# Optimization experiments

Hardware: AMD Instinct MI355X
Metric: run time of the kernel (lower is better)

## Reference

```python
import jax, jax.numpy as jnp
import numpy as np

DIM = 1024
MEM_DIM = 1024
BANK = 8192
B, S = 4, 4096
LN_EPS = 1e-5


def setup_inputs() -> dict:
    key = jax.random.key(0)
    ks = jax.random.split(key, 8)
    std_q = 1.0 / np.sqrt(DIM)
    std_m = 1.0 / np.sqrt(MEM_DIM)
    std_f = 1.0 / np.sqrt(DIM + MEM_DIM)
    return {
        "x": jax.random.normal(ks[0], (B, S, DIM), jnp.float32),
        "knowledge_bank": 0.02 * jax.random.normal(ks[1], (BANK, MEM_DIM), jnp.float32),
        "wq": std_q * jax.random.normal(ks[2], (MEM_DIM, DIM), jnp.float32),
        "bq": jnp.zeros((MEM_DIM,), jnp.float32),
        "wk": std_m * jax.random.normal(ks[3], (MEM_DIM, MEM_DIM), jnp.float32),
        "bk": jnp.zeros((MEM_DIM,), jnp.float32),
        "wv": std_m * jax.random.normal(ks[4], (DIM, MEM_DIM), jnp.float32),
        "bv": jnp.zeros((DIM,), jnp.float32),
        "wf": std_f * jax.random.normal(ks[5], (DIM, DIM + MEM_DIM), jnp.float32),
        "bf": jnp.zeros((DIM,), jnp.float32),
        "gamma": jnp.ones((DIM,), jnp.float32),
        "beta": jnp.zeros((DIM,), jnp.float32),
    }


def reference(x, knowledge_bank, wq, bq, wk, bk, wv, bv, wf, bf, gamma, beta):
    # queries: [B,S,MEM_DIM]; keys/values over the fixed bank: [BANK, *]
    queries = jnp.einsum("bsd,md->bsm", x, wq) + bq
    keys = jnp.einsum("nd,md->nm", knowledge_bank, wk) + bk
    values = jnp.einsum("nd,md->nm", knowledge_bank, wv) + bv
    scores = jnp.einsum("bsm,nm->bsn", queries, keys) / jnp.sqrt(
        jnp.asarray(MEM_DIM, x.dtype)
    )
    attn = jax.nn.softmax(scores, axis=-1)  # [B,S,BANK]
    retrieved = jnp.einsum("bsn,nd->bsd", attn, values)  # [B,S,DIM]
    combined = jnp.concatenate([x, retrieved], axis=-1)  # [B,S,2*DIM]
    out = jnp.einsum("bsc,dc->bsd", combined, wf) + bf
    h = out + x
    # LayerNorm over last dim, eps = 1e-5 (torch default)
    mu = jnp.mean(h, axis=-1, keepdims=True)
    var = jnp.mean(jnp.square(h - mu), axis=-1, keepdims=True)
    return (h - mu) * jax.lax.rsqrt(var + LN_EPS) * gamma + beta
```

## Files before the change

### kernel.cpp

```cpp
#include <hip/hip_runtime.h>


typedef __bf16 bf16;
typedef __bf16 bf16x4 __attribute__((ext_vector_type(4)));
typedef __bf16 bf16x8 __attribute__((ext_vector_type(8)));
typedef float f32x4 __attribute__((ext_vector_type(4)));

static __device__ __forceinline__ f32x4 mfma16(bf16x8 a, bf16x8 b, f32x4 c) {
  return __builtin_amdgcn_mfma_f32_16x16x32_bf16(a, b, c, 0, 0, 0);
}

#define GLDS16(gp, lp) __builtin_amdgcn_global_load_lds( \
    (const __attribute__((address_space(1))) void*)(gp), \
    (__attribute__((address_space(3))) void*)(lp), 16, 0, 0)

static __device__ __forceinline__ void xcd_swizzle(long& bm, long& bn) {
  const int nwg = (int)(gridDim.x * gridDim.y);
  int flat = (int)(blockIdx.y * gridDim.x + blockIdx.x);
  flat = (flat & 7) * (nwg >> 3) + (flat >> 3);
  bm = (long)(flat / (int)gridDim.x) * 128;
  bn = (long)(flat % (int)gridDim.x) * 128;
}

template<int EPI, int CONCAT>
__global__ __launch_bounds__(256, 3) void gemm_bb(
    const bf16* __restrict__ A, const bf16* __restrict__ A2,
    const bf16* __restrict__ W, const float* __restrict__ bias,
    const float* __restrict__ resid, float* __restrict__ L,
    void* __restrict__ Cout, int N, int K, int ldw)
{
  __shared__ bf16 As[128 * 64];
  __shared__ bf16 Bs[128 * 64];
  const int tid = threadIdx.x, lane = tid & 63, wid = tid >> 6;
  const int wm = (wid >> 1) * 64, wn = (wid & 1) * 64;
  const int quad = lane >> 4, l16 = lane & 15;
  long bm, bn;
  xcd_swizzle(bm, bn);

  int prow[4], pcg[4];
#pragma unroll
  for (int i = 0; i < 4; ++i) {
    int p = ((wid * 4 + i) << 6) + lane;
    prow[i] = p >> 3;
    pcg[i] = (p & 7) ^ (prow[i] & 7);
  }

  f32x4 acc[4][4] = {};

  for (int k0 = 0; k0 < K; k0 += 64) {
    const bf16* Asrc = (CONCAT && k0 >= 1024) ? A2 : A;
    const int kA = (CONCAT && k0 >= 1024) ? k0 - 1024 : k0;
    const int lda = CONCAT ? 1024 : K;
    __syncthreads();
#pragma unroll
    for (int i = 0; i < 4; ++i) {
      const bf16* ga = Asrc + (size_t)(bm + prow[i]) * lda + kA + pcg[i] * 8;
      GLDS16(ga, (char*)As + ((wid * 4 + i) << 10));
    }
#pragma unroll
    for (int i = 0; i < 4; ++i) {
      const bf16* gb = W + (size_t)(bn + prow[i]) * ldw + k0 + pcg[i] * 8;
      GLDS16(gb, (char*)Bs + ((wid * 4 + i) << 10));
    }
    __syncthreads();
#pragma unroll
    for (int kk = 0; kk < 2; ++kk) {
      bf16x8 af[4], bfv[4];
#pragma unroll
      for (int mt = 0; mt < 4; ++mt) {
        const int r = wm + mt * 16 + l16;
        af[mt] = *(const bf16x8*)((const char*)As + (r << 7)
                                  + ((((kk << 2) + quad) ^ (r & 7)) << 4));
      }
#pragma unroll
      for (int nt = 0; nt < 4; ++nt) {
        const int r = wn + nt * 16 + l16;
        bfv[nt] = *(const bf16x8*)((const char*)Bs + (r << 7)
                                   + ((((kk << 2) + quad) ^ (r & 7)) << 4));
      }
#pragma unroll
      for (int mt = 0; mt < 4; ++mt)
#pragma unroll
        for (int nt = 0; nt < 4; ++nt)
          acc[mt][nt] = mfma16(af[mt], bfv[nt], acc[mt][nt]);
    }
  }

#pragma unroll
  for (int mt = 0; mt < 4; ++mt) {
    const long row0 = bm + wm + mt * 16 + quad * 4;
    if (EPI == 2) {
      float rsum[4] = {0.f, 0.f, 0.f, 0.f};
#pragma unroll
      for (int nt = 0; nt < 4; ++nt) {
        const long col = bn + wn + nt * 16 + l16;
#pragma unroll
        for (int r = 0; r < 4; ++r) {
          float p = __expf(acc[mt][nt][r] * 0.03125f);
          rsum[r] += p;
          ((bf16*)Cout)[(size_t)(row0 + r) * N + col] = (bf16)p;
        }
      }
#pragma unroll
      for (int s = 1; s < 16; s <<= 1)
#pragma unroll
        for (int r = 0; r < 4; ++r) rsum[r] += __shfl_xor(rsum[r], s, 64);
      if (l16 == 0) {
#pragma unroll
        for (int r = 0; r < 4; ++r) atomicAdd(&L[row0 + r], rsum[r]);
      }
    } else {
#pragma unroll
      for (int nt = 0; nt < 4; ++nt) {
        const long col = bn + wn + nt * 16 + l16;
        const float bc = (EPI == 1) ? 0.f : bias[col];
#pragma unroll
        for (int r = 0; r < 4; ++r) {
          float v = acc[mt][nt][r] + ((EPI == 1) ? bias[row0 + r] : bc);
          if (EPI == 3) {
            v += resid[(size_t)(row0 + r) * 1024 + col];
            ((float*)Cout)[(size_t)(row0 + r) * N + col] = v;
          } else {
            ((bf16*)Cout)[(size_t)(row0 + r) * N + col] = (bf16)v;
          }
        }
      }
    }
  }
}

__global__ __launch_bounds__(512, 2) void pv_gemm(
    const bf16* __restrict__ P, const bf16* __restrict__ Vt,
    const float* __restrict__ L, bf16* __restrict__ Rb)
{
  __shared__ bf16 As[2][128 * 128];
  __shared__ bf16 Bs[2][128 * 128];
  const int tid = threadIdx.x, lane = tid & 63, wid = tid >> 6;
  const int wm = (wid & 3) * 32, wn = (wid >> 2) * 64;
  const int quad = lane >> 4, l16 = lane & 15;
  long bm, bn;
  xcd_swizzle(bm, bn);

  int prow[4], pcg[4];
#pragma unroll
  for (int i = 0; i < 4; ++i) {
    int p = ((wid * 4 + i) << 6) + lane;
    prow[i] = p >> 4;
    pcg[i] = (p & 15) ^ (prow[i] & 15);
  }

  f32x4 acc[2][4] = {};

  auto stage = [&](int buf, int k0) {
#pragma unroll
    for (int i = 0; i < 4; ++i)
      GLDS16(P + (size_t)(bm + prow[i]) * 8192 + k0 + pcg[i] * 8,
             (char*)As[buf] + ((wid * 4 + i) << 10));
#pragma unroll
    for (int i = 0; i < 4; ++i)
      GLDS16(Vt + (size_t)(bn + prow[i]) * 8192 + k0 + pcg[i] * 8,
             (char*)Bs[buf] + ((wid * 4 + i) << 10));
  };

  auto compute = [&](int buf) {
    __builtin_amdgcn_s_setprio(1);
#pragma unroll
    for (int kk = 0; kk < 4; ++kk) {
      bf16x8 af[2], bfv[4];
#pragma unroll
      for (int mt = 0; mt < 2; ++mt) {
        const int r = wm + mt * 16 + l16;
        af[mt] = *(const bf16x8*)((const char*)As[buf] + (r << 8)
                                  + ((((kk << 2) + quad) ^ (r & 15)) << 4));
      }
#pragma unroll
      for (int nt = 0; nt < 4; ++nt) {
        const int r = wn + nt * 16 + l16;
        bfv[nt] = *(const bf16x8*)((const char*)Bs[buf] + (r << 8)
                                   + ((((kk << 2) + quad) ^ (r & 15)) << 4));
      }
#pragma unroll
      for (int mt = 0; mt < 2; ++mt)
#pragma unroll
        for (int nt = 0; nt < 4; ++nt)
          acc[mt][nt] = mfma16(af[mt], bfv[nt], acc[mt][nt]);
    }
    __builtin_amdgcn_s_setprio(0);
  };

  stage(0, 0);
  __syncthreads();
  int cur = 0;
  for (int t = 0; t < 63; ++t) {
    stage(cur ^ 1, (t + 1) * 128);
    compute(cur);
    __syncthreads();
    cur ^= 1;
  }
  compute(cur);

#pragma unroll
  for (int mt = 0; mt < 2; ++mt) {
    const long row0 = bm + wm + mt * 16 + quad * 4;
    float linv[4];
#pragma unroll
    for (int r = 0; r < 4; ++r) linv[r] = 1.f / L[row0 + r];
#pragma unroll
    for (int nt = 0; nt < 4; ++nt) {
      const long col = bn + wn + nt * 16 + l16;
#pragma unroll
      for (int r = 0; r < 4; ++r)
        Rb[(size_t)(row0 + r) * 1024 + col] = (bf16)(acc[mt][nt][r] * linv[r]);
    }
  }
}

template<int BIAS_ROW, int OUT_F32_RES, int CONCAT>
__global__ __launch_bounds__(256, 3) void gemm_nt(
    const float* __restrict__ A, const bf16* __restrict__ A2,
    const float* __restrict__ W, const float* __restrict__ bias,
    const float* __restrict__ resid, void* __restrict__ Cout,
    int M, int N, int K)
{
  __shared__ bf16 As[128][72];
  __shared__ bf16 Bs[128][72];
  const int tid  = threadIdx.x;
  const int lane = tid & 63;
  const int wid  = tid >> 6;
  const int wm   = (wid >> 1) * 64, wn = (wid & 1) * 64;
  const int quad = lane >> 4, l16 = lane & 15;
  const long bm = (long)blockIdx.y * 128, bn = (long)blockIdx.x * 128;
  const int r0 = tid >> 2, cq = (tid & 3) * 16;
  const int lda = CONCAT ? 1024 : K;

  f32x4 acc[4][4] = {};

  for (int k0 = 0; k0 < K; k0 += 64) {
    const bool useb = CONCAT && (k0 >= 1024);
    const int kA = useb ? (k0 - 1024) : k0;
    f32x4 va[2][4], vb[2][4];
    bf16x8 ra[2][2];
    if (useb) {
#pragma unroll
      for (int g = 0; g < 2; ++g) {
        const bf16* p = A2 + (size_t)(bm + r0 + 64 * g) * 1024 + kA + cq;
        ra[g][0] = *(const bf16x8*)p;
        ra[g][1] = *(const bf16x8*)(p + 8);
      }
    } else {
#pragma unroll
      for (int g = 0; g < 2; ++g) {
        const f32x4* p = (const f32x4*)(A + (size_t)(bm + r0 + 64 * g) * lda + kA + cq);
#pragma unroll
        for (int j = 0; j < 4; ++j) va[g][j] = p[j];
      }
    }
#pragma unroll
    for (int g = 0; g < 2; ++g) {
      const f32x4* p = (const f32x4*)(W + (size_t)(bn + r0 + 64 * g) * K + k0 + cq);
#pragma unroll
      for (int j = 0; j < 4; ++j) vb[g][j] = p[j];
    }
    __syncthreads();
#pragma unroll
    for (int g = 0; g < 2; ++g) {
      bf16* dA = &As[r0 + 64 * g][cq];
      if (useb) {
        *(bf16x8*)dA = ra[g][0]; *(bf16x8*)(dA + 8) = ra[g][1];
      } else {
        bf16x8 t0, t1;
#pragma unroll
        for (int j = 0; j < 4; ++j) {
          t0[j] = (bf16)va[g][0][j]; t0[4 + j] = (bf16)va[g][1][j];
          t1[j] = (bf16)va[g][2][j]; t1[4 + j] = (bf16)va[g][3][j];
        }
        *(bf16x8*)dA = t0; *(bf16x8*)(dA + 8) = t1;
      }
      bf16* dB = &Bs[r0 + 64 * g][cq];
      bf16x8 u0, u1;
#pragma unroll
      for (int j = 0; j < 4; ++j) {
        u0[j] = (bf16)vb[g][0][j]; u0[4 + j] = (bf16)vb[g][1][j];
        u1[j] = (bf16)vb[g][2][j]; u1[4 + j] = (bf16)vb[g][3][j];
      }
      *(bf16x8*)dB = u0; *(bf16x8*)(dB + 8) = u1;
    }
    __syncthreads();
#pragma unroll
    for (int kk = 0; kk < 2; ++kk) {
      bf16x8 af[4], bfv[4];
#pragma unroll
      for (int mt = 0; mt < 4; ++mt)
        af[mt] = *(const bf16x8*)&As[wm + mt * 16 + l16][kk * 32 + quad * 8];
#pragma unroll
      for (int nt = 0; nt < 4; ++nt)
        bfv[nt] = *(const bf16x8*)&Bs[wn + nt * 16 + l16][kk * 32 + quad * 8];
#pragma unroll
      for (int mt = 0; mt < 4; ++mt)
#pragma unroll
        for (int nt = 0; nt < 4; ++nt)
          acc[mt][nt] = mfma16(af[mt], bfv[nt], acc[mt][nt]);
    }
  }
#pragma unroll
  for (int mt = 0; mt < 4; ++mt) {
    const long row0 = bm + wm + mt * 16 + quad * 4;
#pragma unroll
    for (int nt = 0; nt < 4; ++nt) {
      const long col = bn + wn + nt * 16 + l16;
      const float bc = BIAS_ROW ? 0.f : bias[col];
#pragma unroll
      for (int r = 0; r < 4; ++r) {
        float v = acc[mt][nt][r] + (BIAS_ROW ? bias[row0 + r] : bc);
        if (OUT_F32_RES) {
          v += resid[(size_t)(row0 + r) * 1024 + col];
          ((float*)Cout)[(size_t)(row0 + r) * N + col] = v;
        } else {
          ((bf16*)Cout)[(size_t)(row0 + r) * N + col] = (bf16)v;
        }
      }
    }
  }
}

__global__ __launch_bounds__(256) void cvt6(
    const float* __restrict__ x, const float* __restrict__ bank,
    const float* __restrict__ wq, const float* __restrict__ wk,
    const float* __restrict__ wv, const float* __restrict__ wf,
    bf16* __restrict__ xb, bf16* __restrict__ bankb,
    bf16* __restrict__ wqb, bf16* __restrict__ wkb,
    bf16* __restrict__ wvb, bf16* __restrict__ wfb)
{
  long i4 = (long)blockIdx.x * 256 + threadIdx.x;
  const float* src; bf16* dst; long off;
  if      (i4 < 4194304) { src = x;    dst = xb;    off = i4; }
  else if (i4 < 6291456) { src = bank; dst = bankb; off = i4 - 4194304; }
  else if (i4 < 6553600) { src = wq;   dst = wqb;   off = i4 - 6291456; }
  else if (i4 < 6815744) { src = wk;   dst = wkb;   off = i4 - 6553600; }
  else if (i4 < 7077888) { src = wv;   dst = wvb;   off = i4 - 6815744; }
  else if (i4 < 7602176) { src = wf;   dst = wfb;   off = i4 - 7077888; }
  else return;
  f32x4 v = ((const f32x4*)src)[off];
  bf16x4 o;
#pragma unroll
  for (int j = 0; j < 4; ++j) o[j] = (bf16)v[j];
  ((bf16x4*)dst)[off] = o;
}

__global__ __launch_bounds__(256) void zerof(float* __restrict__ p) {
  p[(size_t)blockIdx.x * 256 + threadIdx.x] = 0.f;
}

__global__ __launch_bounds__(256) void ln_kernel(
    float* __restrict__ h, const float* __restrict__ g, const float* __restrict__ b)
{
  const int tid = threadIdx.x;
  const size_t row = blockIdx.x;
  f32x4 v = *(f32x4*)&h[row * 1024 + tid * 4];
  float s1 = v[0] + v[1] + v[2] + v[3];
  float s2 = v[0]*v[0] + v[1]*v[1] + v[2]*v[2] + v[3]*v[3];
#pragma unroll
  for (int d = 1; d < 64; d <<= 1) { s1 += __shfl_xor(s1, d, 64); s2 += __shfl_xor(s2, d, 64); }
  __shared__ float a1[4], a2[4];
  const int wid = tid >> 6;
  if ((tid & 63) == 0) { a1[wid] = s1; a2[wid] = s2; }
  __syncthreads();
  s1 = a1[0] + a1[1] + a1[2] + a1[3];
  s2 = a2[0] + a2[1] + a2[2] + a2[3];
  const float mu = s1 * (1.f / 1024.f);
  const float rs = rsqrtf(s2 * (1.f / 1024.f) - mu * mu + 1e-5f);
  f32x4 gv = *(const f32x4*)&g[tid * 4];
  f32x4 bv = *(const f32x4*)&b[tid * 4];
#pragma unroll
  for (int j = 0; j < 4; ++j) v[j] = (v[j] - mu) * rs * gv[j] + bv[j];
  *(f32x4*)&h[row * 1024 + tid * 4] = v;
}

extern "C" void kernel_launch(void* const* d_in, const int* in_sizes, int n_in,
                              void* d_out, int out_size, void* d_ws, size_t ws_size,
                              hipStream_t stream)
{
  const float* x     = (const float*)d_in[0];
  const float* kbank = (const float*)d_in[1];
  const float* wq    = (const float*)d_in[2];
  const float* bq    = (const float*)d_in[3];
  const float* wk    = (const float*)d_in[4];
  const float* bk    = (const float*)d_in[5];
  const float* wv    = (const float*)d_in[6];
  const float* bv    = (const float*)d_in[7];
  const float* wf    = (const float*)d_in[8];
  const float* bf_   = (const float*)d_in[9];
  const float* gamma = (const float*)d_in[10];
  const float* beta  = (const float*)d_in[11];

  char* ws = (char*)d_ws;
  const size_t MB = 1024 * 1024;
  bf16*  Qb    = (bf16*)ws;
  bf16*  Rb    = Qb;
  bf16*  Kb    = (bf16*)(ws + 32 * MB);
  bf16*  Vt    = (bf16*)(ws + 48 * MB);
  float* L     = (float*)(ws + 64 * MB);
  bf16*  xb    = (bf16*)(ws + 65 * MB);
  bf16*  bankb = (bf16*)(ws + 97 * MB);
  bf16*  wfb   = (bf16*)(ws + 113 * MB);
  bf16*  wqb   = (bf16*)(ws + 117 * MB);
  bf16*  wkb   = (bf16*)(ws + 119 * MB);
  bf16*  wvb   = (bf16*)(ws + 121 * MB);
  bf16*  P     = (bf16*)d_out;
  float* out   = (float*)d_out;
  const bool big = ws_size >= 123 * MB;

  if (big) {
    cvt6<<<dim3(29696), dim3(256), 0, stream>>>(
        x, kbank, wq, wk, wv, wf, xb, bankb, wqb, wkb, wvb, wfb);
    gemm_bb<0,0><<<dim3(8, 128), dim3(256), 0, stream>>>(
        xb, nullptr, wqb, bq, nullptr, nullptr, (void*)Qb, 1024, 1024, 1024);
    gemm_bb<0,0><<<dim3(8, 64), dim3(256), 0, stream>>>(
        bankb, nullptr, wkb, bk, nullptr, nullptr, (void*)Kb, 1024, 1024, 1024);
    gemm_bb<1,0><<<dim3(64, 8), dim3(256), 0, stream>>>(
        wvb, nullptr, bankb, bv, nullptr, nullptr, (void*)Vt, 8192, 1024, 1024);
  } else {
    gemm_nt<0,0,0><<<dim3(8, 128), dim3(256), 0, stream>>>(
        x, nullptr, wq, bq, nullptr, (void*)Qb, 16384, 1024, 1024);
    gemm_nt<0,0,0><<<dim3(8, 64), dim3(256), 0, stream>>>(
        kbank, nullptr, wk, bk, nullptr, (void*)Kb, 8192, 1024, 1024);
    gemm_nt<1,0,0><<<dim3(64, 8), dim3(256), 0, stream>>>(
        wv, nullptr, kbank, bv, nullptr, (void*)Vt, 1024, 8192, 1024);
  }

  zerof<<<dim3(64), dim3(256), 0, stream>>>(L);
  for (int c = 0; c < 4; ++c) {
    if (big)
      gemm_bb<2,0><<<dim3(64, 32), dim3(256), 0, stream>>>(
          Qb + (size_t)c * 4096 * 1024, nullptr, Kb, nullptr, nullptr,
          L + c * 4096, (void*)P, 8192, 1024, 1024);
    else
      gemm_bb<2,0><<<dim3(64, 32), dim3(256), 0, stream>>>(
          Qb + (size_t)c * 4096 * 1024, nullptr, Kb, nullptr, nullptr,
          L + c * 4096, (void*)P, 8192, 1024, 1024);
    pv_gemm<<<dim3(8, 32), dim3(512), 0, stream>>>(
        P, Vt, L + c * 4096, Rb + (size_t)c * 4096 * 1024);
  }

  if (big) {
    gemm_bb<3,1><<<dim3(8, 128), dim3(256), 0, stream>>>(
        xb, Rb, wfb, bf_, x, nullptr, (void*)out, 1024, 2048, 2048);
  } else {
    gemm_nt<0,1,1><<<dim3(8, 128), dim3(256), 0, stream>>>(
        x, Rb, wf, bf_, x, (void*)out, 16384, 1024, 2048);
  }
  ln_kernel<<<dim3(16384), dim3(256), 0, stream>>>(out, gamma, beta);
}
```

Before: 1.087 ms.

## Deepen PV GEMM pipeline to four stages and remap blocks to XCDs

The PV GEMM switches from double-buffered 128-wide K tiles to four 64-wide K buffers with three loads in flight. Each step waits only on the oldest load via explicit vmcnt waits and raw barriers, so global-to-LDS loads overlap compute more. A new XCD mapping for the QK^T and Vt GEMMs gives each XCD a contiguous column slice of the N dimension, which is meant to improve L2 reuse of the shared operand. The trade-offs are halved K per compute step, more barriers, and reliance on exact vmcnt counting.

```diff
diff --git a/kernel.cpp b/kernel.cpp
--- a/kernel.cpp
+++ b/kernel.cpp
@@ -14,15 +14,7 @@
     (const __attribute__((address_space(1))) void*)(gp), \
     (__attribute__((address_space(3))) void*)(lp), 16, 0, 0)
 
-static __device__ __forceinline__ void xcd_swizzle(long& bm, long& bn) {
-  const int nwg = (int)(gridDim.x * gridDim.y);
-  int flat = (int)(blockIdx.y * gridDim.x + blockIdx.x);
-  flat = (flat & 7) * (nwg >> 3) + (flat >> 3);
-  bm = (long)(flat / (int)gridDim.x) * 128;
-  bn = (long)(flat % (int)gridDim.x) * 128;
-}
-
-template<int EPI, int CONCAT>
+template<int EPI, int CONCAT, int XMAP>
 __global__ __launch_bounds__(256, 3) void gemm_bb(
     const bf16* __restrict__ A, const bf16* __restrict__ A2,
     const bf16* __restrict__ W, const float* __restrict__ bias,
@@ -35,7 +27,22 @@
   const int wm = (wid >> 1) * 64, wn = (wid & 1) * 64;
   const int quad = lane >> 4, l16 = lane & 15;
   long bm, bn;
-  xcd_swizzle(bm, bn);
+  if (XMAP == 1) {
+    const int flat = (int)(blockIdx.y * gridDim.x + blockIdx.x);
+    const int xcd = flat & 7;
+    const int idx = flat >> 3;
+    const int nbxl = (int)gridDim.x >> 3;
+    const int byp = idx / nbxl;
+    const int bxl = idx - byp * nbxl;
+    bm = (long)byp * 128;
+    bn = (long)(xcd * nbxl + bxl) * 128;
+  } else {
+    const int nwg = (int)(gridDim.x * gridDim.y);
+    int flat = (int)(blockIdx.y * gridDim.x + blockIdx.x);
+    flat = (flat & 7) * (nwg >> 3) + (flat >> 3);
+    bm = (long)(flat / (int)gridDim.x) * 128;
+    bn = (long)(flat % (int)gridDim.x) * 128;
+  }
 
   int prow[4], pcg[4];
 #pragma unroll
@@ -133,51 +140,57 @@
     const bf16* __restrict__ P, const bf16* __restrict__ Vt,
     const float* __restrict__ L, bf16* __restrict__ Rb)
 {
-  __shared__ bf16 As[2][128 * 128];
-  __shared__ bf16 Bs[2][128 * 128];
+  __shared__ bf16 As[4][128 * 64];
+  __shared__ bf16 Bs[4][128 * 64];
   const int tid = threadIdx.x, lane = tid & 63, wid = tid >> 6;
   const int wm = (wid & 3) * 32, wn = (wid >> 2) * 64;
   const int quad = lane >> 4, l16 = lane & 15;
   long bm, bn;
-  xcd_swizzle(bm, bn);
-
-  int prow[4], pcg[4];
-#pragma unroll
-  for (int i = 0; i < 4; ++i) {
-    int p = ((wid * 4 + i) << 6) + lane;
-    prow[i] = p >> 4;
-    pcg[i] = (p & 15) ^ (prow[i] & 15);
+  {
+    const int nwg = (int)(gridDim.x * gridDim.y);
+    int flat = (int)(blockIdx.y * gridDim.x + blockIdx.x);
+    flat = (flat & 7) * (nwg >> 3) + (flat >> 3);
+    bm = (long)(flat / (int)gridDim.x) * 128;
+    bn = (long)(flat % (int)gridDim.x) * 128;
+  }
+
+  int prow[2], pcg[2];
+#pragma unroll
+  for (int i = 0; i < 2; ++i) {
+    int p = ((wid * 2 + i) << 6) + lane;
+    prow[i] = p >> 3;
+    pcg[i] = (p & 7) ^ (prow[i] & 7);
   }
 
   f32x4 acc[2][4] = {};
 
   auto stage = [&](int buf, int k0) {
 #pragma unroll
-    for (int i = 0; i < 4; ++i)
+    for (int i = 0; i < 2; ++i)
       GLDS16(P + (size_t)(bm + prow[i]) * 8192 + k0 + pcg[i] * 8,
-             (char*)As[buf] + ((wid * 4 + i) << 10));
-#pragma unroll
-    for (int i = 0; i < 4; ++i)
+             (char*)As[buf] + ((wid * 2 + i) << 10));
+#pragma unroll
+    for (int i = 0; i < 2; ++i)
       GLDS16(Vt + (size_t)(bn + prow[i]) * 8192 + k0 + pcg[i] * 8,
-             (char*)Bs[buf] + ((wid * 4 + i) << 10));
+             (char*)Bs[buf] + ((wid * 2 + i) << 10));
   };
 
   auto compute = [&](int buf) {
     __builtin_amdgcn_s_setprio(1);
 #pragma unroll
-    for (int kk = 0; kk < 4; ++kk) {
+    for (int kk = 0; kk < 2; ++kk) {
       bf16x8 af[2], bfv[4];
 #pragma unroll
       for (int mt = 0; mt < 2; ++mt) {
         const int r = wm + mt * 16 + l16;
-        af[mt] = *(const bf16x8*)((const char*)As[buf] + (r << 8)
-                                  + ((((kk << 2) + quad) ^ (r & 15)) << 4));
+        af[mt] = *(const bf16x8*)((const char*)As[buf] + (r << 7)
+                                  + ((((kk << 2) + quad) ^ (r & 7)) << 4));
       }
 #pragma unroll
       for (int nt = 0; nt < 4; ++nt) {
         const int r = wn + nt * 16 + l16;
-        bfv[nt] = *(const bf16x8*)((const char*)Bs[buf] + (r << 8)
-                                   + ((((kk << 2) + quad) ^ (r & 15)) << 4));
+        bfv[nt] = *(const bf16x8*)((const char*)Bs[buf] + (r << 7)
+                                   + ((((kk << 2) + quad) ^ (r & 7)) << 4));
       }
 #pragma unroll
       for (int mt = 0; mt < 2; ++mt)
@@ -189,15 +202,20 @@
   };
 
   stage(0, 0);
-  __syncthreads();
-  int cur = 0;
-  for (int t = 0; t < 63; ++t) {
-    stage(cur ^ 1, (t + 1) * 128);
-    compute(cur);
-    __syncthreads();
-    cur ^= 1;
-  }
-  compute(cur);
+  stage(1, 64);
+  stage(2, 128);
+  for (int t = 0; t < 126; ++t) {
+    asm volatile("s_waitcnt vmcnt(8)" ::: "memory");
+    __builtin_amdgcn_s_barrier();
+    compute(t & 3);
+    if (t < 125) stage((t + 3) & 3, (t + 3) * 64);
+  }
+  asm volatile("s_waitcnt vmcnt(4)" ::: "memory");
+  __builtin_amdgcn_s_barrier();
+  compute(126 & 3);
+  asm volatile("s_waitcnt vmcnt(0)" ::: "memory");
+  __builtin_amdgcn_s_barrier();
+  compute(127 & 3);
 
 #pragma unroll
   for (int mt = 0; mt < 2; ++mt) {
@@ -413,11 +431,11 @@
   if (big) {
     cvt6<<<dim3(29696), dim3(256), 0, stream>>>(
         x, kbank, wq, wk, wv, wf, xb, bankb, wqb, wkb, wvb, wfb);
-    gemm_bb<0,0><<<dim3(8, 128), dim3(256), 0, stream>>>(
+    gemm_bb<0,0,0><<<dim3(8, 128), dim3(256), 0, stream>>>(
         xb, nullptr, wqb, bq, nullptr, nullptr, (void*)Qb, 1024, 1024, 1024);
-    gemm_bb<0,0><<<dim3(8, 64), dim3(256), 0, stream>>>(
+    gemm_bb<0,0,0><<<dim3(8, 64), dim3(256), 0, stream>>>(
         bankb, nullptr, wkb, bk, nullptr, nullptr, (void*)Kb, 1024, 1024, 1024);
-    gemm_bb<1,0><<<dim3(64, 8), dim3(256), 0, stream>>>(
+    gemm_bb<1,0,1><<<dim3(64, 8), dim3(256), 0, stream>>>(
         wvb, nullptr, bankb, bv, nullptr, nullptr, (void*)Vt, 8192, 1024, 1024);
   } else {
     gemm_nt<0,0,0><<<dim3(8, 128), dim3(256), 0, stream>>>(
@@ -430,20 +448,15 @@
 
   zerof<<<dim3(64), dim3(256), 0, stream>>>(L);
   for (int c = 0; c < 4; ++c) {
-    if (big)
-      gemm_bb<2,0><<<dim3(64, 32), dim3(256), 0, stream>>>(
-          Qb + (size_t)c * 4096 * 1024, nullptr, Kb, nullptr, nullptr,
-          L + c * 4096, (void*)P, 8192, 1024, 1024);
-    else
-      gemm_bb<2,0><<<dim3(64, 32), dim3(256), 0, stream>>>(
-          Qb + (size_t)c * 4096 * 1024, nullptr, Kb, nullptr, nullptr,
-          L + c * 4096, (void*)P, 8192, 1024, 1024);
+    gemm_bb<2,0,1><<<dim3(64, 32), dim3(256), 0, stream>>>(
+        Qb + (size_t)c * 4096 * 1024, nullptr, Kb, nullptr, nullptr,
+        L + c * 4096, (void*)P, 8192, 1024, 1024);
     pv_gemm<<<dim3(8, 32), dim3(512), 0, stream>>>(
         P, Vt, L + c * 4096, Rb + (size_t)c * 4096 * 1024);
   }
 
   if (big) {
-    gemm_bb<3,1><<<dim3(8, 128), dim3(256), 0, stream>>>(
+    gemm_bb<3,1,0><<<dim3(8, 128), dim3(256), 0, stream>>>(
         xb, Rb, wfb, bf_, x, nullptr, (void*)out, 1024, 2048, 2048);
   } else {
     gemm_nt<0,1,1><<<dim3(8, 128), dim3(256), 0, stream>>>(
```

Measured after the change: 1.018 ms. -6.3%, faster.
